# Performance work log

Measured on AMD Instinct MI355X. Metric: run time of the kernel, lower is better.

The kernel has to match this reference:

```python
import jax, jax.numpy as jnp
import numpy as np

B, S, E, H = 2, 2048, 2048, 16
D = E // H  # head_dim = 128
EPS = 1e-5


def setup_inputs() -> dict:
    key = jax.random.key(0)
    ks = jax.random.split(key, 16)
    s_e = 1.0 / np.sqrt(E)
    s_f = 1.0 / np.sqrt(4 * E)
    return {
        "x": jax.random.normal(ks[0], (B, S, E), jnp.float32),
        "ln1_w": jnp.ones((E,), jnp.float32) + 0.01 * jax.random.normal(ks[1], (E,)),
        "ln1_b": 0.01 * jax.random.normal(ks[2], (E,)),
        "wq": s_e * jax.random.normal(ks[3], (E, E), jnp.float32),
        "wk": s_e * jax.random.normal(ks[4], (E, E), jnp.float32),
        "wv": s_e * jax.random.normal(ks[5], (E, E), jnp.float32),
        "wo": s_e * jax.random.normal(ks[6], (E, E), jnp.float32),
        "bo": 0.01 * jax.random.normal(ks[7], (E,)),
        "ln2_w": jnp.ones((E,), jnp.float32) + 0.01 * jax.random.normal(ks[8], (E,)),
        "ln2_b": 0.01 * jax.random.normal(ks[9], (E,)),
        "w1": s_e * jax.random.normal(ks[10], (E, 4 * E), jnp.float32),
        "b1": 0.01 * jax.random.normal(ks[11], (4 * E,)),
        "w2": s_f * jax.random.normal(ks[12], (4 * E, E), jnp.float32),
        "b2": 0.01 * jax.random.normal(ks[13], (E,)),
    }


def _layernorm(x, w, b):
    mu = jnp.mean(x, axis=-1, keepdims=True)
    var = jnp.var(x, axis=-1, keepdims=True)
    return (x - mu) * jax.lax.rsqrt(var + EPS) * w + b


def _attention(x, wq, wk, wv, wo, bo):
    # x: [B,S,E] -> q,k,v: [B,H,S,D]
    def split(t):
        return t.reshape(B, S, H, D).transpose(0, 2, 1, 3)
    q = split(x @ wq)
    k = split(x @ wk)
    v = split(x @ wv)
    scores = jnp.einsum("bhqd,bhkd->bhqk", q, k)  # [B,H,S,S]
    causal = jnp.triu(jnp.ones((S, S), bool), k=1)
    scores = jnp.where(causal, -jnp.inf, scores)
    # NOTE: faithful to source -- scaling applied after masking, inside softmax arg
    attn = jax.nn.softmax(scores / np.sqrt(D), axis=-1)
    ctx = jnp.einsum("bhqk,bhkd->bhqd", attn, v)
    ctx = ctx.transpose(0, 2, 1, 3).reshape(B, S, E)
    return ctx @ wo + bo


def reference(x, ln1_w, ln1_b, wq, wk, wv, wo, bo, ln2_w, ln2_b, w1, b1, w2, b2):
    shortcut = x
    x1 = _layernorm(x, ln1_w, ln1_b)
    attn_out = _attention(x1, wq, wk, wv, wo, bo)
    a = attn_out + shortcut
    # NOTE: faithful to source quirk -- second shortcut is post-LN1 x1, not a
    y = _layernorm(a, ln2_w, ln2_b)
    y = jax.nn.gelu(y @ w1 + b1, approximate=False) @ w2 + b2
    return x1 + y
```

## Files before the change

kernel.cpp:

```cpp
#include <hip/hip_runtime.h>
#include <math.h>

typedef unsigned short u16;
typedef unsigned int u32;
typedef __attribute__((ext_vector_type(8))) short short8;
typedef __attribute__((ext_vector_type(4))) float f32x4;
typedef __attribute__((ext_vector_type(16))) float f32x16;
typedef __attribute__((ext_vector_type(4))) u32 u32x4;
typedef __attribute__((ext_vector_type(2))) u32 u32x2;

#define DEVFN static __device__ __forceinline__

DEVFN u16 f2bf(float x) {
  union { float f; u32 u; } v; v.f = x;
  u32 r = v.u + 0x7fffu + ((v.u >> 16) & 1u);
  return (u16)(r >> 16);
}
DEVFN float bf2f(u16 h) {
  union { u32 u; float f; } v; v.u = ((u32)h) << 16;
  return v.f;
}
DEVFN u32 packbf2(float a, float b) {
  return (u32)f2bf(a) | ((u32)f2bf(b) << 16);
}
DEVFN void gl2lds16(const u16* g, u16* l) {
  __builtin_amdgcn_global_load_lds(
      (const __attribute__((address_space(1))) u32*)g,
      (__attribute__((address_space(3))) u32*)l, 16, 0, 0);
}
DEVFN float gelu_exact(float v) {
  float s = v * 0.70710678118654752f;
  float ax = fabsf(s);
  float t = __builtin_amdgcn_rcpf(1.0f + 0.3275911f * ax);
  float poly = t * (0.254829592f +
               t * (-0.284496736f +
               t * (1.421413741f +
               t * (-1.453152027f + t * 1.061405429f))));
  float e = __expf(-s * s);
  float er = 1.0f - poly * e;
  er = (s < 0.f) ? -er : er;
  return 0.5f * v * (1.0f + er);
}

__global__ __launch_bounds__(256) void tconv_k(const float* __restrict__ in,
                                               u16* __restrict__ out, int K, int N) {
  __shared__ float tile[32][33];
  int n0 = blockIdx.x << 5, k0 = blockIdx.y << 5;
  int tx = threadIdx.x & 31, ty = threadIdx.x >> 5;
#pragma unroll
  for (int i = 0; i < 32; i += 8)
    tile[ty + i][tx] = in[(long)(k0 + ty + i) * N + n0 + tx];
  __syncthreads();
#pragma unroll
  for (int i = 0; i < 32; i += 8)
    out[(long)(n0 + ty + i) * K + k0 + tx] = f2bf(tile[tx][ty + i]);
}

__global__ __launch_bounds__(256) void ln1_k(const float* __restrict__ x,
                                             const float* __restrict__ w,
                                             const float* __restrict__ b,
                                             float* __restrict__ y32,
                                             u16* __restrict__ y16) {
  long base = (long)blockIdx.x * 2048;
  int t = threadIdx.x;
  float4 v0 = ((const float4*)(x + base))[2 * t];
  float4 v1 = ((const float4*)(x + base))[2 * t + 1];
  float xv[8];
  *(float4*)xv = v0; *(float4*)(xv + 4) = v1;
  float s = 0.f, ss = 0.f;
#pragma unroll
  for (int i = 0; i < 8; ++i) { s += xv[i]; ss += xv[i] * xv[i]; }
#pragma unroll
  for (int m = 1; m < 64; m <<= 1) { s += __shfl_xor(s, m); ss += __shfl_xor(ss, m); }
  __shared__ float rs[4], rss[4];
  int wave = t >> 6;
  if ((t & 63) == 0) { rs[wave] = s; rss[wave] = ss; }
  __syncthreads();
  s = rs[0] + rs[1] + rs[2] + rs[3];
  ss = rss[0] + rss[1] + rss[2] + rss[3];
  float mean = s * (1.f / 2048.f);
  float var = ss * (1.f / 2048.f) - mean * mean;
  float inv = rsqrtf(var + 1e-5f);
  float wv[8], bv[8];
  *(float4*)wv = ((const float4*)w)[2 * t]; *(float4*)(wv + 4) = ((const float4*)w)[2 * t + 1];
  *(float4*)bv = ((const float4*)b)[2 * t]; *(float4*)(bv + 4) = ((const float4*)b)[2 * t + 1];
  float yv[8];
#pragma unroll
  for (int i = 0; i < 8; ++i) yv[i] = (xv[i] - mean) * inv * wv[i] + bv[i];
  ((float4*)(y32 + base))[2 * t] = *(float4*)yv;
  ((float4*)(y32 + base))[2 * t + 1] = *(float4*)(yv + 4);
  u32x4 ov;
#pragma unroll
  for (int i = 0; i < 4; ++i) ov[i] = packbf2(yv[2 * i], yv[2 * i + 1]);
  ((u32x4*)(y16 + base))[t] = ov;
}

__global__ __launch_bounds__(256) void ln2_k(const u16* __restrict__ a,
                                             const float* __restrict__ w,
                                             const float* __restrict__ b,
                                             u16* __restrict__ y) {
  long base = (long)blockIdx.x * 2048;
  int t = threadIdx.x;
  u32x4 pv = ((const u32x4*)(a + base))[t];
  float xv[8];
#pragma unroll
  for (int i = 0; i < 4; ++i) {
    xv[2 * i] = bf2f((u16)(pv[i] & 0xffffu));
    xv[2 * i + 1] = bf2f((u16)(pv[i] >> 16));
  }
  float s = 0.f, ss = 0.f;
#pragma unroll
  for (int i = 0; i < 8; ++i) { s += xv[i]; ss += xv[i] * xv[i]; }
#pragma unroll
  for (int m = 1; m < 64; m <<= 1) { s += __shfl_xor(s, m); ss += __shfl_xor(ss, m); }
  __shared__ float rs[4], rss[4];
  int wave = t >> 6;
  if ((t & 63) == 0) { rs[wave] = s; rss[wave] = ss; }
  __syncthreads();
  s = rs[0] + rs[1] + rs[2] + rs[3];
  ss = rss[0] + rss[1] + rss[2] + rss[3];
  float mean = s * (1.f / 2048.f);
  float var = ss * (1.f / 2048.f) - mean * mean;
  float inv = rsqrtf(var + 1e-5f);
  float wv[8], bv[8];
  *(float4*)wv = ((const float4*)w)[2 * t]; *(float4*)(wv + 4) = ((const float4*)w)[2 * t + 1];
  *(float4*)bv = ((const float4*)b)[2 * t]; *(float4*)(bv + 4) = ((const float4*)b)[2 * t + 1];
  u32x4 ov;
#pragma unroll
  for (int i = 0; i < 4; ++i) {
    float y0 = (xv[2 * i] - mean) * inv * wv[2 * i] + bv[2 * i];
    float y1 = (xv[2 * i + 1] - mean) * inv * wv[2 * i + 1] + bv[2 * i + 1];
    ov[i] = packbf2(y0, y1);
  }
  ((u32x4*)(y + base))[t] = ov;
}

#define VMW6() asm volatile("s_waitcnt vmcnt(6)" ::: "memory")
#define VMW0() asm volatile("s_waitcnt vmcnt(0)" ::: "memory")
#define CFENCE() asm volatile("" ::: "memory")
#define BARRIER() do { CFENCE(); __builtin_amdgcn_s_barrier(); CFENCE(); } while (0)

template <int MODE>
__global__ __launch_bounds__(512, 2) void gemm3_k(const u16* __restrict__ A,
                                                  const u16* __restrict__ W,
                                                  void* __restrict__ outp,
                                                  const float* __restrict__ bias,
                                                  const float* __restrict__ resid,
                                                  int M, int N, int K) {
  __shared__ __align__(16) u16 lds[3][24576];
  const int t = threadIdx.x, lane = t & 63, wave = t >> 6;
  const int g = lane >> 4, r16 = lane & 15;
  const int wm = wave >> 2, wn = wave & 3;
  const int nM = M >> 7;
  const int nwg = gridDim.x * gridDim.y;
  const int orig = blockIdx.y * gridDim.x + blockIdx.x;
  const int sw = (nwg & 7) ? orig : ((orig & 7) * (nwg >> 3) + (orig >> 3));
  const long m0 = (long)(sw % nM) * 128, n0 = (long)(sw / nM) * 256;
  const int nt = K >> 6;
  const long Kl = K;
  const int rl = lane >> 3, cc = lane & 7;

  auto stA = [&](u16* Lb, long tile) {
#pragma unroll
    for (int q = 0; q < 2; ++q) {
      int rr = (wave * 2 + q) * 8 + rl;
      int c = cc ^ (rr & 7);
      gl2lds16(A + (m0 + rr) * Kl + (tile << 6) + c * 8, Lb + (wave * 2 + q) * 512);
    }
  };
  auto stB = [&](u16* Lb, int half, long tile) {
#pragma unroll
    for (int q = 0; q < 2; ++q) {
      int rr = (wave * 2 + q) * 8 + rl;
      int c = cc ^ (rr & 7);
      gl2lds16(W + (n0 + half * 128 + rr) * Kl + (tile << 6) + c * 8,
               Lb + 8192 + half * 8192 + (wave * 2 + q) * 512);
    }
  };

  f32x4 acc[4][4] = {};
  u16* L0 = &lds[0][0];
  u16* L1 = &lds[1][0];
  u16* L2 = &lds[2][0];

  stA(L0, 0); stB(L0, 0, 0); stB(L0, 1, 0);
  if (nt > 1) { stA(L1, 1); stB(L1, 0, 1); stB(L1, 1, 1); }
  if (nt > 2) { VMW6(); } else { VMW0(); }
  BARRIER();

  for (int tt = 0; tt < nt; ++tt) {
    const long ts = (tt + 2 < nt) ? (long)(tt + 2) : (long)(nt - 1);
    short8 af[4][2], bf[2][2];
#pragma unroll
    for (int ii2 = 0; ii2 < 4; ++ii2) {
      int row = (ii2 * 2 + wm) * 16 + r16;
#pragma unroll
      for (int kk = 0; kk < 2; ++kk)
        af[ii2][kk] = *(const short8*)(L0 + row * 64 + (((kk << 2) | g) ^ (row & 7)) * 8);
    }
#pragma unroll
    for (int jj2 = 0; jj2 < 2; ++jj2) {
      int row = (jj2 * 4 + wn) * 16 + r16;
#pragma unroll
      for (int kk = 0; kk < 2; ++kk)
        bf[jj2][kk] = *(const short8*)(L0 + 8192 + row * 64 + (((kk << 2) | g) ^ (row & 7)) * 8);
    }
    stA(L2, ts); stB(L2, 0, ts);
    __builtin_amdgcn_s_setprio(1);
#pragma unroll
    for (int ii2 = 0; ii2 < 4; ++ii2)
#pragma unroll
      for (int jj2 = 0; jj2 < 2; ++jj2)
#pragma unroll
        for (int kk = 0; kk < 2; ++kk)
          acc[ii2][jj2] = __builtin_amdgcn_mfma_f32_16x16x32_bf16(
              af[ii2][kk], bf[jj2][kk], acc[ii2][jj2], 0, 0, 0);
    __builtin_amdgcn_s_setprio(0);
    BARRIER();
#pragma unroll
    for (int jj2 = 0; jj2 < 2; ++jj2) {
      int row = ((2 + jj2) * 4 + wn) * 16 + r16;
#pragma unroll
      for (int kk = 0; kk < 2; ++kk)
        bf[jj2][kk] = *(const short8*)(L0 + 8192 + row * 64 + (((kk << 2) | g) ^ (row & 7)) * 8);
    }
    stB(L2, 1, ts);
    __builtin_amdgcn_s_setprio(1);
#pragma unroll
    for (int ii2 = 0; ii2 < 4; ++ii2)
#pragma unroll
      for (int jj2 = 0; jj2 < 2; ++jj2)
#pragma unroll
        for (int kk = 0; kk < 2; ++kk)
          acc[ii2][2 + jj2] = __builtin_amdgcn_mfma_f32_16x16x32_bf16(
              af[ii2][kk], bf[jj2][kk], acc[ii2][2 + jj2], 0, 0, 0);
    __builtin_amdgcn_s_setprio(0);
    VMW6(); BARRIER();
    u16* tmp = L0; L0 = L1; L1 = L2; L2 = tmp;
  }
  VMW0();

  const long Nl = N;
#pragma unroll
  for (int ii = 0; ii < 4; ++ii) {
#pragma unroll
    for (int jj = 0; jj < 4; ++jj) {
#pragma unroll
      for (int r = 0; r < 4; ++r) {
        long mg = m0 + (ii * 2 + wm) * 16 + g * 4 + r;
        long ng = n0 + (jj * 4 + wn) * 16 + r16;
        float v = acc[ii][jj][r];
        if constexpr (MODE == 0) {
          int which = (int)(n0 >> 11);
          long nloc = ng & 2047;
          long bb = mg >> 11, sq = mg & 2047;
          long hh = nloc >> 7, dd = nloc & 127;
          long idx = (which < 2) ? (((bb * 16 + hh) * 2048 + sq) * 128 + dd)
                                 : (((bb * 16 + hh) * 128 + dd) * 2048 + sq);
          ((u16*)outp)[(long)which * 8388608 + idx] = f2bf(v);
        } else if constexpr (MODE == 2) {
          v += bias[ng] + resid[mg * Nl + ng];
          ((u16*)outp)[mg * Nl + ng] = f2bf(v);
        } else if constexpr (MODE == 3) {
          v = gelu_exact(v + bias[ng]);
          ((u16*)outp)[mg * Nl + ng] = f2bf(v);
        } else {
          v += bias[ng] + resid[mg * Nl + ng];
          ((float*)outp)[mg * Nl + ng] = v;
        }
      }
    }
  }
}

__global__ __launch_bounds__(256, 2) void attn2_k(const u16* __restrict__ Qp,
                                                  const u16* __restrict__ Kp,
                                                  const u16* __restrict__ Vp,
                                                  u16* __restrict__ ctx) {
  __shared__ __align__(16) u16 KsL[2][64 * 128];
  __shared__ __align__(16) u16 VsL[2][128 * 64];
  const int qt = gridDim.x - 1 - blockIdx.x;
  const int bh = blockIdx.y;
  const int t = threadIdx.x, lane = t & 63, wave = t >> 6;
  const int l31 = lane & 31, hi = lane >> 5;
  const int q0 = qt * 128, qw0 = q0 + wave * 32;
  const int qg = qw0 + l31;
  const u16* Qh = Qp + (long)bh * 2048 * 128;
  const u16* Kh = Kp + (long)bh * 2048 * 128;
  const u16* Vh = Vp + (long)bh * 128 * 2048;
  const int nkt = qt * 2 + 2;
  const int ktmax = (qw0 + 31) >> 6;
  const float cs = 0.12753042923810058f;

  short8 qf[8];
#pragma unroll
  for (int ds = 0; ds < 8; ++ds)
    qf[ds] = *(const short8*)(Qh + (long)qg * 128 + ds * 16 + hi * 8);

  f32x16 O0 = {}, O1 = {}, O2 = {}, O3 = {};
  float m = -INFINITY, l = 0.f;

  auto stage = [&](int b, int kt) {
#pragma unroll
    for (int q = 0; q < 4; ++q) {
      int r = wave * 16 + q * 4 + (lane >> 4);
      int c = (lane & 15) ^ (r & 15);
      gl2lds16(Kh + ((long)kt * 64 + r) * 128 + c * 8,
               &KsL[b][(wave * 16 + q * 4) * 128]);
    }
#pragma unroll
    for (int q = 0; q < 4; ++q) {
      int r = wave * 32 + q * 8 + (lane >> 3);
      int c = (lane & 7) ^ (r & 7);
      gl2lds16(Vh + (long)r * 2048 + kt * 64 + c * 8,
               &VsL[b][(wave * 32 + q * 8) * 64]);
    }
  };

  stage(0, 0);
  VMW0(); BARRIER();

  for (int kt = 0; kt < nkt; ++kt) {
    const int cur = kt & 1;
    if (kt + 1 < nkt) stage(cur ^ 1, kt + 1);
    if (kt <= ktmax) {
      f32x16 S0 = {}, S1 = {};
      __builtin_amdgcn_s_setprio(1);
#pragma unroll
      for (int ds = 0; ds < 8; ++ds) {
        int c0 = ((ds * 2 + hi) ^ (l31 & 15)) * 8;
        short8 k0 = *(const short8*)(&KsL[cur][l31 * 128 + c0]);
        int r1 = 32 + l31;
        int c1 = ((ds * 2 + hi) ^ (r1 & 15)) * 8;
        short8 k1 = *(const short8*)(&KsL[cur][r1 * 128 + c1]);
        S0 = __builtin_amdgcn_mfma_f32_32x32x16_bf16(k0, qf[ds], S0, 0, 0, 0);
        S1 = __builtin_amdgcn_mfma_f32_32x32x16_bf16(k1, qf[ds], S1, 0, 0, 0);
      }
      __builtin_amdgcn_s_setprio(0);
      float p[32];
#pragma unroll
      for (int i = 0; i < 16; ++i) { p[i] = S0[i]; p[16 + i] = S1[i]; }
      if (kt * 64 + 63 > qw0) {
#pragma unroll
        for (int ks = 0; ks < 2; ++ks)
#pragma unroll
          for (int r = 0; r < 16; ++r) {
            int kg = kt * 64 + ks * 32 + (r & 3) + 8 * (r >> 2) + 4 * hi;
            if (kg > qg) p[ks * 16 + r] = -INFINITY;
          }
      }
      float tmax = p[0];
#pragma unroll
      for (int i = 1; i < 32; ++i) tmax = fmaxf(tmax, p[i]);
      tmax = fmaxf(tmax, __shfl_xor(tmax, 32));
      float mnew = fmaxf(m, tmax);
      float corr = __builtin_amdgcn_exp2f((m - mnew) * cs);
      float ls = 0.f;
#pragma unroll
      for (int i = 0; i < 32; ++i) {
        p[i] = __builtin_amdgcn_exp2f((p[i] - mnew) * cs);
        ls += p[i];
      }
      ls += __shfl_xor(ls, 32);
      l = l * corr + ls;
      m = mnew;
#pragma unroll
      for (int i = 0; i < 16; ++i) {
        O0[i] *= corr; O1[i] *= corr; O2[i] *= corr; O3[i] *= corr;
      }
      short8 pf[4];
#pragma unroll
      for (int gg = 0; gg < 4; ++gg) {
        u32 u_, v_, w_, z_;
        asm("v_cvt_pk_bf16_f32 %0, %1, %2" : "=v"(u_) : "v"(p[gg * 8 + 0]), "v"(p[gg * 8 + 1]));
        asm("v_cvt_pk_bf16_f32 %0, %1, %2" : "=v"(v_) : "v"(p[gg * 8 + 2]), "v"(p[gg * 8 + 3]));
        asm("v_cvt_pk_bf16_f32 %0, %1, %2" : "=v"(w_) : "v"(p[gg * 8 + 4]), "v"(p[gg * 8 + 5]));
        asm("v_cvt_pk_bf16_f32 %0, %1, %2" : "=v"(z_) : "v"(p[gg * 8 + 6]), "v"(p[gg * 8 + 7]));
        asm("v_permlane32_swap_b32 %0, %1" : "+v"(u_), "+v"(w_));
        asm("v_permlane32_swap_b32 %0, %1" : "+v"(v_), "+v"(z_));
        union { u32 w4[4]; short8 s; } cv;
        cv.w4[0] = u_; cv.w4[1] = v_; cv.w4[2] = w_; cv.w4[3] = z_;
        pf[gg] = cv.s;
      }
      __builtin_amdgcn_s_setprio(1);
#define PVROW(ds, OO)                                                          \
  {                                                                            \
    int row = (ds)*32 + l31;                                                   \
    _Pragma("unroll") for (int gg = 0; gg < 4; ++gg) {                         \
      short8 vf = *(const short8*)(&VsL[cur][row * 64 +                        \
                                             (((gg * 2 + hi) ^ (row & 7)) * 8)]); \
      OO = __builtin_amdgcn_mfma_f32_32x32x16_bf16(vf, pf[gg], OO, 0, 0, 0);   \
    }                                                                          \
  }
      PVROW(0, O0); PVROW(1, O1); PVROW(2, O2); PVROW(3, O3);
#undef PVROW
      __builtin_amdgcn_s_setprio(0);
    }
    VMW0(); BARRIER();
  }

  const float inv = 1.f / l;
  u16* cp = ctx + ((long)(bh >> 4) * 2048 + qg) * 2048 + (bh & 15) * 128;
#define WROUT(OO, dsb)                                                         \
  _Pragma("unroll") for (int rg = 0; rg < 4; ++rg) {                           \
    int d = (dsb)*32 + 8 * rg + 4 * hi;                                        \
    u32x2 wv;                                                                  \
    wv[0] = packbf2(OO[4 * rg] * inv, OO[4 * rg + 1] * inv);                   \
    wv[1] = packbf2(OO[4 * rg + 2] * inv, OO[4 * rg + 3] * inv);               \
    *(u32x2*)(cp + d) = wv;                                                    \
  }
  WROUT(O0, 0); WROUT(O1, 1); WROUT(O2, 2); WROUT(O3, 3);
#undef WROUT
}

extern "C" void kernel_launch(void* const* d_in, const int* in_sizes, int n_in,
                              void* d_out, int out_size, void* d_ws, size_t ws_size,
                              hipStream_t stream) {
  const float* x = (const float*)d_in[0];
  const float* ln1w = (const float*)d_in[1];
  const float* ln1b = (const float*)d_in[2];
  const float* wq = (const float*)d_in[3];
  const float* wk = (const float*)d_in[4];
  const float* wv = (const float*)d_in[5];
  const float* wo = (const float*)d_in[6];
  const float* bo = (const float*)d_in[7];
  const float* ln2w = (const float*)d_in[8];
  const float* ln2b = (const float*)d_in[9];
  const float* w1 = (const float*)d_in[10];
  const float* b1 = (const float*)d_in[11];
  const float* w2 = (const float*)d_in[12];
  const float* b2 = (const float*)d_in[13];
  float* out = (float*)d_out;
  char* ws = (char*)d_ws;

  float* x1f = (float*)(ws + 0);
  u16* x1b = (u16*)(ws + 33554432);
  u16* wqt = (u16*)(ws + 50331648);
  u16* wkt = (u16*)(ws + 58720256);
  u16* wvt = (u16*)(ws + 67108864);
  u16* wot = (u16*)(ws + 75497472);
  u16* w1t = (u16*)(ws + 83886080);
  u16* w2t = (u16*)(ws + 117440512);
  u16* qb = (u16*)(ws + 150994944);
  u16* kb = (u16*)(ws + 167772160);
  u16* vb = (u16*)(ws + 184549376);
  u16* ctxb = (u16*)(ws + 201326592);
  u16* ab = (u16*)(ws + 218103808);
  u16* y0b = (u16*)(ws + 234881024);
  u16* hb = qb;

  tconv_k<<<dim3(64, 64), 256, 0, stream>>>(wq, wqt, 2048, 2048);
  tconv_k<<<dim3(64, 64), 256, 0, stream>>>(wk, wkt, 2048, 2048);
  tconv_k<<<dim3(64, 64), 256, 0, stream>>>(wv, wvt, 2048, 2048);
  tconv_k<<<dim3(64, 64), 256, 0, stream>>>(wo, wot, 2048, 2048);
  tconv_k<<<dim3(256, 64), 256, 0, stream>>>(w1, w1t, 2048, 8192);
  tconv_k<<<dim3(64, 256), 256, 0, stream>>>(w2, w2t, 8192, 2048);
  ln1_k<<<4096, 256, 0, stream>>>(x, ln1w, ln1b, x1f, x1b);
  gemm3_k<0><<<dim3(32, 24), 512, 0, stream>>>(x1b, wqt, qb, nullptr, nullptr, 4096, 6144, 2048);
  attn2_k<<<dim3(16, 32), 256, 0, stream>>>(qb, kb, vb, ctxb);
  gemm3_k<2><<<dim3(32, 8), 512, 0, stream>>>(ctxb, wot, ab, bo, x, 4096, 2048, 2048);
  ln2_k<<<4096, 256, 0, stream>>>(ab, ln2w, ln2b, y0b);
  gemm3_k<3><<<dim3(32, 32), 512, 0, stream>>>(y0b, w1t, hb, b1, nullptr, 4096, 8192, 2048);
  gemm3_k<4><<<dim3(32, 8), 512, 0, stream>>>(hb, w2t, out, b2, x1f, 4096, 2048, 8192);
}
```

Measured before the change: 664.8 us.

## Add 256x256-tile double-buffered GEMM and split-K for FFN down projection

Introduces a new GEMM kernel with 256x256 output tiles, double-buffered LDS (64KB per stage) and swizzled direct global-to-LDS loads. It is used for the QKV projection and the FFN up projection. The FFN down projection now uses split-K by two into fp32 partial buffers, followed by a separate reduction kernel that adds bias and residual. Larger tiles raise arithmetic intensity and split-K gives the small-N GEMM enough workgroups. The cost is an extra pass over the partials, more workspace traffic, and possibly lower occupancy from the larger LDS footprint.

```diff
diff --git a/kernel.cpp b/kernel.cpp
--- a/kernel.cpp
+++ b/kernel.cpp
@@ -41,6 +41,14 @@
   er = (s < 0.f) ? -er : er;
   return 0.5f * v * (1.0f + er);
 }
+
+#define VMW8() asm volatile("s_waitcnt vmcnt(8)" ::: "memory")
+#define VMW6() asm volatile("s_waitcnt vmcnt(6)" ::: "memory")
+#define VMW2() asm volatile("s_waitcnt vmcnt(2)" ::: "memory")
+#define VMW0() asm volatile("s_waitcnt vmcnt(0)" ::: "memory")
+#define LGKM0() asm volatile("s_waitcnt lgkmcnt(0)" ::: "memory")
+#define CFENCE() asm volatile("" ::: "memory")
+#define BARRIER() do { CFENCE(); __builtin_amdgcn_s_barrier(); CFENCE(); } while (0)
 
 __global__ __launch_bounds__(256) void tconv_k(const float* __restrict__ in,
                                                u16* __restrict__ out, int K, int N) {
@@ -135,10 +143,149 @@
   ((u32x4*)(y + base))[t] = ov;
 }
 
-#define VMW6() asm volatile("s_waitcnt vmcnt(6)" ::: "memory")
-#define VMW0() asm volatile("s_waitcnt vmcnt(0)" ::: "memory")
-#define CFENCE() asm volatile("" ::: "memory")
-#define BARRIER() do { CFENCE(); __builtin_amdgcn_s_barrier(); CFENCE(); } while (0)
+template <int MODE>
+__global__ __launch_bounds__(512, 2) void gemm2x_k(const u16* __restrict__ A,
+                                                   const u16* __restrict__ W,
+                                                   void* __restrict__ outp,
+                                                   const float* __restrict__ bias) {
+  constexpr int nM = 16;
+  constexpr int nN = (MODE == 0) ? 24 : (MODE == 3) ? 32 : 8;
+  constexpr int KS = (MODE == 5) ? 2 : 1;
+  constexpr int KK = (MODE == 5) ? 4096 : 2048;
+  constexpr long LD = (MODE == 5) ? 8192 : 2048;
+  constexpr int nt = KK / 64;
+  constexpr int nwg = nM * nN * KS;
+  __shared__ __align__(16) u16 lds[2][32768];
+  const int t = threadIdx.x, lane = t & 63, wave = t >> 6;
+  const int g = lane >> 4, r16 = lane & 15;
+  const int wm = wave >> 2, wn = wave & 3;
+  const int orig = blockIdx.y * gridDim.x + blockIdx.x;
+  const int sw = (orig & 7) * (nwg >> 3) + (orig >> 3);
+  const int mi = sw % nM;
+  const int rest = sw / nM;
+  const int ni = (MODE == 5) ? (rest & 7) : rest;
+  const int ks = (MODE == 5) ? (rest >> 3) : 0;
+  const long m0 = (long)mi * 256, n0 = (long)ni * 256;
+  const long k0 = (long)ks * 4096;
+  const int rl = lane >> 3, cl = lane & 7;
+
+  auto stA = [&](int b, int half, int tile) {
+#pragma unroll
+    for (int q = 0; q < 2; ++q) {
+      int rr = (wave * 2 + q) * 8 + rl;
+      gl2lds16(A + (m0 + half * 128 + rr) * LD + k0 + (long)tile * 64 + (cl ^ (rr & 7)) * 8,
+               &lds[b][half * 8192 + (wave * 2 + q) * 512]);
+    }
+  };
+  auto stB = [&](int b, int half, int tile) {
+#pragma unroll
+    for (int q = 0; q < 2; ++q) {
+      int rr = (wave * 2 + q) * 8 + rl;
+      gl2lds16(W + (n0 + half * 128 + rr) * LD + k0 + (long)tile * 64 + (cl ^ (rr & 7)) * 8,
+               &lds[b][16384 + half * 8192 + (wave * 2 + q) * 512]);
+    }
+  };
+
+  f32x4 acc[8][4] = {};
+  stA(0, 0, 0); stA(0, 1, 0); stB(0, 0, 0); stB(0, 1, 0);
+  stA(1, 0, 1); stA(1, 1, 1); stB(1, 0, 1); stB(1, 1, 1);
+
+  for (int tt = 0; tt < nt; ++tt) {
+    const int cur = tt & 1;
+    const u16* Lc = &lds[cur][0];
+    VMW8();
+    BARRIER();
+    short8 a0[8], b0[4];
+#pragma unroll
+    for (int ii = 0; ii < 8; ++ii) {
+      int row = wm * 128 + ii * 16 + r16;
+      a0[ii] = *(const short8*)(Lc + row * 64 + (g ^ (row & 7)) * 8);
+    }
+#pragma unroll
+    for (int jj = 0; jj < 4; ++jj) {
+      int row = wn * 64 + jj * 16 + r16;
+      b0[jj] = *(const short8*)(Lc + 16384 + row * 64 + (g ^ (row & 7)) * 8);
+    }
+    __builtin_amdgcn_s_setprio(1);
+#pragma unroll
+    for (int ii = 0; ii < 8; ++ii)
+#pragma unroll
+      for (int jj = 0; jj < 4; ++jj)
+        acc[ii][jj] = __builtin_amdgcn_mfma_f32_16x16x32_bf16(a0[ii], b0[jj], acc[ii][jj], 0, 0, 0);
+    __builtin_amdgcn_s_setprio(0);
+    short8 a1[8], b1f[4];
+#pragma unroll
+    for (int ii = 0; ii < 8; ++ii) {
+      int row = wm * 128 + ii * 16 + r16;
+      a1[ii] = *(const short8*)(Lc + row * 64 + ((4 | g) ^ (row & 7)) * 8);
+    }
+#pragma unroll
+    for (int jj = 0; jj < 4; ++jj) {
+      int row = wn * 64 + jj * 16 + r16;
+      b1f[jj] = *(const short8*)(Lc + 16384 + row * 64 + ((4 | g) ^ (row & 7)) * 8);
+    }
+    LGKM0();
+    BARRIER();
+    {
+      const int ts = (tt + 2 < nt) ? tt + 2 : nt - 1;
+      stA(cur, 0, ts); stA(cur, 1, ts); stB(cur, 0, ts); stB(cur, 1, ts);
+    }
+    __builtin_amdgcn_s_setprio(1);
+#pragma unroll
+    for (int ii = 0; ii < 8; ++ii)
+#pragma unroll
+      for (int jj = 0; jj < 4; ++jj)
+        acc[ii][jj] = __builtin_amdgcn_mfma_f32_16x16x32_bf16(a1[ii], b1f[jj], acc[ii][jj], 0, 0, 0);
+    __builtin_amdgcn_s_setprio(0);
+  }
+  VMW0();
+
+#pragma unroll
+  for (int ii = 0; ii < 8; ++ii) {
+#pragma unroll
+    for (int jj = 0; jj < 4; ++jj) {
+#pragma unroll
+      for (int r = 0; r < 4; ++r) {
+        long mg = m0 + wm * 128 + ii * 16 + g * 4 + r;
+        long ng = n0 + wn * 64 + jj * 16 + r16;
+        float v = acc[ii][jj][r];
+        if constexpr (MODE == 0) {
+          long which = ng >> 11;
+          long nloc = ng & 2047;
+          long bb = mg >> 11, sq = mg & 2047;
+          long hh = nloc >> 7, dd = nloc & 127;
+          long idx = (which < 2) ? (((bb * 16 + hh) * 2048 + sq) * 128 + dd)
+                                 : (((bb * 16 + hh) * 128 + dd) * 2048 + sq);
+          ((u16*)outp)[which * 8388608 + idx] = f2bf(v);
+        } else if constexpr (MODE == 3) {
+          v = gelu_exact(v + bias[ng]);
+          ((u16*)outp)[mg * 8192 + ng] = f2bf(v);
+        } else {
+          ((float*)outp)[(long)ks * 8388608 + mg * 2048 + ng] = v;
+        }
+      }
+    }
+  }
+}
+
+__global__ __launch_bounds__(256) void red_k(const float* __restrict__ p,
+                                             const float* __restrict__ bias,
+                                             const float* __restrict__ resid,
+                                             float* __restrict__ out) {
+  long i = (long)blockIdx.x * 256 + threadIdx.x;
+  for (long idx = i; idx < 2097152; idx += 2048 * 256) {
+    float4 a = ((const float4*)p)[idx];
+    float4 b = ((const float4*)(p + 8388608))[idx];
+    float4 r = ((const float4*)resid)[idx];
+    float4 bs = ((const float4*)bias)[idx & 511];
+    float4 o;
+    o.x = a.x + b.x + r.x + bs.x;
+    o.y = a.y + b.y + r.y + bs.y;
+    o.z = a.z + b.z + r.z + bs.z;
+    o.w = a.w + b.w + r.w + bs.w;
+    ((float4*)out)[idx] = o;
+  }
+}
 
 template <int MODE>
 __global__ __launch_bounds__(512, 2) void gemm3_k(const u16* __restrict__ A,
@@ -250,19 +397,8 @@
         long mg = m0 + (ii * 2 + wm) * 16 + g * 4 + r;
         long ng = n0 + (jj * 4 + wn) * 16 + r16;
         float v = acc[ii][jj][r];
-        if constexpr (MODE == 0) {
-          int which = (int)(n0 >> 11);
-          long nloc = ng & 2047;
-          long bb = mg >> 11, sq = mg & 2047;
-          long hh = nloc >> 7, dd = nloc & 127;
-          long idx = (which < 2) ? (((bb * 16 + hh) * 2048 + sq) * 128 + dd)
-                                 : (((bb * 16 + hh) * 128 + dd) * 2048 + sq);
-          ((u16*)outp)[(long)which * 8388608 + idx] = f2bf(v);
-        } else if constexpr (MODE == 2) {
+        if constexpr (MODE == 2) {
           v += bias[ng] + resid[mg * Nl + ng];
-          ((u16*)outp)[mg * Nl + ng] = f2bf(v);
-        } else if constexpr (MODE == 3) {
-          v = gelu_exact(v + bias[ng]);
           ((u16*)outp)[mg * Nl + ng] = f2bf(v);
         } else {
           v += bias[ng] + resid[mg * Nl + ng];
@@ -448,6 +584,7 @@
   u16* ab = (u16*)(ws + 218103808);
   u16* y0b = (u16*)(ws + 234881024);
   u16* hb = qb;
+  float* pbuf = (float*)(ws + 50331648);
 
   tconv_k<<<dim3(64, 64), 256, 0, stream>>>(wq, wqt, 2048, 2048);
   tconv_k<<<dim3(64, 64), 256, 0, stream>>>(wk, wkt, 2048, 2048);
@@ -456,10 +593,11 @@
   tconv_k<<<dim3(256, 64), 256, 0, stream>>>(w1, w1t, 2048, 8192);
   tconv_k<<<dim3(64, 256), 256, 0, stream>>>(w2, w2t, 8192, 2048);
   ln1_k<<<4096, 256, 0, stream>>>(x, ln1w, ln1b, x1f, x1b);
-  gemm3_k<0><<<dim3(32, 24), 512, 0, stream>>>(x1b, wqt, qb, nullptr, nullptr, 4096, 6144, 2048);
+  gemm2x_k<0><<<dim3(16, 24), 512, 0, stream>>>(x1b, wqt, qb, nullptr);
   attn2_k<<<dim3(16, 32), 256, 0, stream>>>(qb, kb, vb, ctxb);
   gemm3_k<2><<<dim3(32, 8), 512, 0, stream>>>(ctxb, wot, ab, bo, x, 4096, 2048, 2048);
   ln2_k<<<4096, 256, 0, stream>>>(ab, ln2w, ln2b, y0b);
-  gemm3_k<3><<<dim3(32, 32), 512, 0, stream>>>(y0b, w1t, hb, b1, nullptr, 4096, 8192, 2048);
-  gemm3_k<4><<<dim3(32, 8), 512, 0, stream>>>(hb, w2t, out, b2, x1f, 4096, 2048, 8192);
-}
+  gemm2x_k<3><<<dim3(16, 32), 512, 0, stream>>>(y0b, w1t, hb, b1);
+  gemm2x_k<5><<<dim3(16, 16), 512, 0, stream>>>(hb, w2t, pbuf, nullptr);
+  red_k<<<2048, 256, 0, stream>>>(pbuf, b2, x1f, out);
+}
```

Result: faster. 644.0 us (-3.1%).

## Replace GEMM with 128x128 double-buffered 32x32 MFMA kernel and fuse weight transposes

Applied to the files above, without the earlier changes.

Replaces the 128x256-tile, 512-thread, triple-buffered GEMM using 16x16x32 MFMAs with a 128x128-tile, 256-thread, double-buffered kernel using 32x32x16 bf16 MFMAs. Grid sizes double to match the smaller tiles. The six weight transpose-convert launches are merged into one kernel. The larger MFMA shape reduces LDS fragment reads per flop, but the smaller tile lowers operand reuse and the simpler two-buffer pipeline waits on all loads every iteration, which exposes more memory latency.

```diff
diff --git a/kernel.cpp b/kernel.cpp
--- a/kernel.cpp
+++ b/kernel.cpp
@@ -42,10 +42,33 @@
   return 0.5f * v * (1.0f + er);
 }
 
-__global__ __launch_bounds__(256) void tconv_k(const float* __restrict__ in,
-                                               u16* __restrict__ out, int K, int N) {
+#define VMW0() asm volatile("s_waitcnt vmcnt(0)" ::: "memory")
+#define CFENCE() asm volatile("" ::: "memory")
+#define BARRIER() do { CFENCE(); __builtin_amdgcn_s_barrier(); CFENCE(); } while (0)
+
+__global__ __launch_bounds__(256) void tconvall_k(
+    const float* __restrict__ wq, const float* __restrict__ wk,
+    const float* __restrict__ wv, const float* __restrict__ wo,
+    const float* __restrict__ w1, const float* __restrict__ w2,
+    u16* __restrict__ wqt, u16* __restrict__ wkt, u16* __restrict__ wvt,
+    u16* __restrict__ wot, u16* __restrict__ w1t, u16* __restrict__ w2t) {
   __shared__ float tile[32][33];
-  int n0 = blockIdx.x << 5, k0 = blockIdx.y << 5;
+  int b = blockIdx.x;
+  const float* in; u16* out; int K, N, tn, tk;
+  if (b < 16384) {
+    int wsel = b >> 12;
+    int loc = b & 4095;
+    in = (wsel == 0) ? wq : (wsel == 1) ? wk : (wsel == 2) ? wv : wo;
+    out = (wsel == 0) ? wqt : (wsel == 1) ? wkt : (wsel == 2) ? wvt : wot;
+    K = 2048; N = 2048; tn = loc & 63; tk = loc >> 6;
+  } else if (b < 32768) {
+    int loc = b - 16384; in = w1; out = w1t; K = 2048; N = 8192;
+    tn = loc & 255; tk = loc >> 8;
+  } else {
+    int loc = b - 32768; in = w2; out = w2t; K = 8192; N = 2048;
+    tn = loc & 63; tk = loc >> 6;
+  }
+  int n0 = tn << 5, k0 = tk << 5;
   int tx = threadIdx.x & 31, ty = threadIdx.x >> 5;
 #pragma unroll
   for (int i = 0; i < 32; i += 8)
@@ -135,129 +158,102 @@
   ((u32x4*)(y + base))[t] = ov;
 }
 
-#define VMW6() asm volatile("s_waitcnt vmcnt(6)" ::: "memory")
-#define VMW0() asm volatile("s_waitcnt vmcnt(0)" ::: "memory")
-#define CFENCE() asm volatile("" ::: "memory")
-#define BARRIER() do { CFENCE(); __builtin_amdgcn_s_barrier(); CFENCE(); } while (0)
-
 template <int MODE>
-__global__ __launch_bounds__(512, 2) void gemm3_k(const u16* __restrict__ A,
+__global__ __launch_bounds__(256, 2) void gemm9_k(const u16* __restrict__ A,
                                                   const u16* __restrict__ W,
                                                   void* __restrict__ outp,
                                                   const float* __restrict__ bias,
                                                   const float* __restrict__ resid,
                                                   int M, int N, int K) {
-  __shared__ __align__(16) u16 lds[3][24576];
+  __shared__ __align__(16) u16 lds[2][16384];
   const int t = threadIdx.x, lane = t & 63, wave = t >> 6;
-  const int g = lane >> 4, r16 = lane & 15;
-  const int wm = wave >> 2, wn = wave & 3;
+  const int l31 = lane & 31, hi = lane >> 5;
+  const int wm = wave >> 1, wn = wave & 1;
   const int nM = M >> 7;
   const int nwg = gridDim.x * gridDim.y;
   const int orig = blockIdx.y * gridDim.x + blockIdx.x;
-  const int sw = (nwg & 7) ? orig : ((orig & 7) * (nwg >> 3) + (orig >> 3));
-  const long m0 = (long)(sw % nM) * 128, n0 = (long)(sw / nM) * 256;
+  const int sw = (orig & 7) * (nwg >> 3) + (orig >> 3);
+  const long m0 = (long)(sw % nM) * 128, n0 = (long)(sw / nM) * 128;
   const int nt = K >> 6;
   const long Kl = K;
-  const int rl = lane >> 3, cc = lane & 7;
-
-  auto stA = [&](u16* Lb, long tile) {
-#pragma unroll
-    for (int q = 0; q < 2; ++q) {
-      int rr = (wave * 2 + q) * 8 + rl;
-      int c = cc ^ (rr & 7);
-      gl2lds16(A + (m0 + rr) * Kl + (tile << 6) + c * 8, Lb + (wave * 2 + q) * 512);
+  const int srow = lane >> 3, schk = lane & 7;
+
+  auto stA = [&](int b, int ts) {
+#pragma unroll
+    for (int q = 0; q < 4; ++q) {
+      int rb = q * 32 + wave * 8;
+      int rr = rb + srow;
+      gl2lds16(A + (m0 + rr) * Kl + (long)ts * 64 + (schk ^ (rr & 7)) * 8,
+               &lds[b][rb * 64]);
     }
   };
-  auto stB = [&](u16* Lb, int half, long tile) {
-#pragma unroll
-    for (int q = 0; q < 2; ++q) {
-      int rr = (wave * 2 + q) * 8 + rl;
-      int c = cc ^ (rr & 7);
-      gl2lds16(W + (n0 + half * 128 + rr) * Kl + (tile << 6) + c * 8,
-               Lb + 8192 + half * 8192 + (wave * 2 + q) * 512);
+  auto stB = [&](int b, int ts) {
+#pragma unroll
+    for (int q = 0; q < 4; ++q) {
+      int rb = q * 32 + wave * 8;
+      int rr = rb + srow;
+      gl2lds16(W + (n0 + rr) * Kl + (long)ts * 64 + (schk ^ (rr & 7)) * 8,
+               &lds[b][8192 + rb * 64]);
     }
   };
 
-  f32x4 acc[4][4] = {};
-  u16* L0 = &lds[0][0];
-  u16* L1 = &lds[1][0];
-  u16* L2 = &lds[2][0];
-
-  stA(L0, 0); stB(L0, 0, 0); stB(L0, 1, 0);
-  if (nt > 1) { stA(L1, 1); stB(L1, 0, 1); stB(L1, 1, 1); }
-  if (nt > 2) { VMW6(); } else { VMW0(); }
-  BARRIER();
+  f32x16 acc[2][2] = {};
+
+  stA(0, 0); stB(0, 0);
 
   for (int tt = 0; tt < nt; ++tt) {
-    const long ts = (tt + 2 < nt) ? (long)(tt + 2) : (long)(nt - 1);
-    short8 af[4][2], bf[2][2];
-#pragma unroll
-    for (int ii2 = 0; ii2 < 4; ++ii2) {
-      int row = (ii2 * 2 + wm) * 16 + r16;
-#pragma unroll
-      for (int kk = 0; kk < 2; ++kk)
-        af[ii2][kk] = *(const short8*)(L0 + row * 64 + (((kk << 2) | g) ^ (row & 7)) * 8);
-    }
-#pragma unroll
-    for (int jj2 = 0; jj2 < 2; ++jj2) {
-      int row = (jj2 * 4 + wn) * 16 + r16;
-#pragma unroll
-      for (int kk = 0; kk < 2; ++kk)
-        bf[jj2][kk] = *(const short8*)(L0 + 8192 + row * 64 + (((kk << 2) | g) ^ (row & 7)) * 8);
-    }
-    stA(L2, ts); stB(L2, 0, ts);
+    const int cur = tt & 1;
+    const int ts = (tt + 1 < nt) ? tt + 1 : tt;
+    VMW0();
+    BARRIER();
+    stA(cur ^ 1, ts); stB(cur ^ 1, ts);
+    const u16* Lc = &lds[cur][0];
+    short8 af[2][4], bf[2][4];
+#pragma unroll
+    for (int i = 0; i < 2; ++i) {
+      int row = wm * 64 + i * 32 + l31;
+#pragma unroll
+      for (int s = 0; s < 4; ++s)
+        af[i][s] = *(const short8*)(Lc + row * 64 + (((s << 1) | hi) ^ (row & 7)) * 8);
+    }
+#pragma unroll
+    for (int j = 0; j < 2; ++j) {
+      int row = wn * 64 + j * 32 + l31;
+#pragma unroll
+      for (int s = 0; s < 4; ++s)
+        bf[j][s] = *(const short8*)(Lc + 8192 + row * 64 + (((s << 1) | hi) ^ (row & 7)) * 8);
+    }
     __builtin_amdgcn_s_setprio(1);
 #pragma unroll
-    for (int ii2 = 0; ii2 < 4; ++ii2)
-#pragma unroll
-      for (int jj2 = 0; jj2 < 2; ++jj2)
-#pragma unroll
-        for (int kk = 0; kk < 2; ++kk)
-          acc[ii2][jj2] = __builtin_amdgcn_mfma_f32_16x16x32_bf16(
-              af[ii2][kk], bf[jj2][kk], acc[ii2][jj2], 0, 0, 0);
+    for (int i = 0; i < 2; ++i)
+#pragma unroll
+      for (int j = 0; j < 2; ++j)
+#pragma unroll
+        for (int s = 0; s < 4; ++s)
+          acc[i][j] = __builtin_amdgcn_mfma_f32_32x32x16_bf16(
+              af[i][s], bf[j][s], acc[i][j], 0, 0, 0);
     __builtin_amdgcn_s_setprio(0);
-    BARRIER();
-#pragma unroll
-    for (int jj2 = 0; jj2 < 2; ++jj2) {
-      int row = ((2 + jj2) * 4 + wn) * 16 + r16;
-#pragma unroll
-      for (int kk = 0; kk < 2; ++kk)
-        bf[jj2][kk] = *(const short8*)(L0 + 8192 + row * 64 + (((kk << 2) | g) ^ (row & 7)) * 8);
-    }
-    stB(L2, 1, ts);
-    __builtin_amdgcn_s_setprio(1);
-#pragma unroll
-    for (int ii2 = 0; ii2 < 4; ++ii2)
-#pragma unroll
-      for (int jj2 = 0; jj2 < 2; ++jj2)
-#pragma unroll
-        for (int kk = 0; kk < 2; ++kk)
-          acc[ii2][2 + jj2] = __builtin_amdgcn_mfma_f32_16x16x32_bf16(
-              af[ii2][kk], bf[jj2][kk], acc[ii2][2 + jj2], 0, 0, 0);
-    __builtin_amdgcn_s_setprio(0);
-    VMW6(); BARRIER();
-    u16* tmp = L0; L0 = L1; L1 = L2; L2 = tmp;
   }
   VMW0();
 
   const long Nl = N;
 #pragma unroll
-  for (int ii = 0; ii < 4; ++ii) {
-#pragma unroll
-    for (int jj = 0; jj < 4; ++jj) {
-#pragma unroll
-      for (int r = 0; r < 4; ++r) {
-        long mg = m0 + (ii * 2 + wm) * 16 + g * 4 + r;
-        long ng = n0 + (jj * 4 + wn) * 16 + r16;
-        float v = acc[ii][jj][r];
+  for (int i = 0; i < 2; ++i) {
+#pragma unroll
+    for (int j = 0; j < 2; ++j) {
+#pragma unroll
+      for (int r = 0; r < 16; ++r) {
+        long mg = m0 + wm * 64 + i * 32 + (r & 3) + 8 * (r >> 2) + 4 * hi;
+        long ng = n0 + wn * 64 + j * 32 + l31;
+        float v = acc[i][j][r];
         if constexpr (MODE == 0) {
-          int which = (int)(n0 >> 11);
+          long which = ng >> 11;
           long nloc = ng & 2047;
           long bb = mg >> 11, sq = mg & 2047;
           long hh = nloc >> 7, dd = nloc & 127;
           long idx = (which < 2) ? (((bb * 16 + hh) * 2048 + sq) * 128 + dd)
                                  : (((bb * 16 + hh) * 128 + dd) * 2048 + sq);
-          ((u16*)outp)[(long)which * 8388608 + idx] = f2bf(v);
+          ((u16*)outp)[which * 8388608 + idx] = f2bf(v);
         } else if constexpr (MODE == 2) {
           v += bias[ng] + resid[mg * Nl + ng];
           ((u16*)outp)[mg * Nl + ng] = f2bf(v);
@@ -449,17 +445,13 @@
   u16* y0b = (u16*)(ws + 234881024);
   u16* hb = qb;
 
-  tconv_k<<<dim3(64, 64), 256, 0, stream>>>(wq, wqt, 2048, 2048);
-  tconv_k<<<dim3(64, 64), 256, 0, stream>>>(wk, wkt, 2048, 2048);
-  tconv_k<<<dim3(64, 64), 256, 0, stream>>>(wv, wvt, 2048, 2048);
-  tconv_k<<<dim3(64, 64), 256, 0, stream>>>(wo, wot, 2048, 2048);
-  tconv_k<<<dim3(256, 64), 256, 0, stream>>>(w1, w1t, 2048, 8192);
-  tconv_k<<<dim3(64, 256), 256, 0, stream>>>(w2, w2t, 8192, 2048);
+  tconvall_k<<<49152, 256, 0, stream>>>(wq, wk, wv, wo, w1, w2,
+                                        wqt, wkt, wvt, wot, w1t, w2t);
   ln1_k<<<4096, 256, 0, stream>>>(x, ln1w, ln1b, x1f, x1b);
-  gemm3_k<0><<<dim3(32, 24), 512, 0, stream>>>(x1b, wqt, qb, nullptr, nullptr, 4096, 6144, 2048);
+  gemm9_k<0><<<dim3(32, 48), 256, 0, stream>>>(x1b, wqt, qb, nullptr, nullptr, 4096, 6144, 2048);
   attn2_k<<<dim3(16, 32), 256, 0, stream>>>(qb, kb, vb, ctxb);
-  gemm3_k<2><<<dim3(32, 8), 512, 0, stream>>>(ctxb, wot, ab, bo, x, 4096, 2048, 2048);
+  gemm9_k<2><<<dim3(32, 16), 256, 0, stream>>>(ctxb, wot, ab, bo, x, 4096, 2048, 2048);
   ln2_k<<<4096, 256, 0, stream>>>(ab, ln2w, ln2b, y0b);
-  gemm3_k<3><<<dim3(32, 32), 512, 0, stream>>>(y0b, w1t, hb, b1, nullptr, 4096, 8192, 2048);
-  gemm3_k<4><<<dim3(32, 8), 512, 0, stream>>>(hb, w2t, out, b2, x1f, 4096, 2048, 8192);
-}
+  gemm9_k<3><<<dim3(32, 64), 256, 0, stream>>>(y0b, w1t, hb, b1, nullptr, 4096, 8192, 2048);
+  gemm9_k<4><<<dim3(32, 16), 256, 0, stream>>>(hb, w2t, out, b2, x1f, 4096, 2048, 8192);
+}
```

Result: slower. 745.2 us (+12.1%).
